# Performance work log

Hardware: AMD Instinct MI355X
Metric: run time of the kernel (lower is better)

The kernel has to match this reference:

```python
import jax, jax.numpy as jnp
import numpy as np

BATCH = 16384
NUM_CLASSES = 1000
FEA_DIM = 1024
MARGIN = 5.0


def setup_inputs() -> dict:
    key = jax.random.key(0)
    k1, k2, k3 = jax.random.split(key, 3)
    x = jax.random.normal(k1, (BATCH, FEA_DIM), dtype=jnp.float32)
    labels = jax.random.randint(k2, (BATCH,), 0, NUM_CLASSES)
    centers = jax.random.normal(k3, (NUM_CLASSES, FEA_DIM), dtype=jnp.float32)
    return {"x": x, "labels": labels, "centers": centers}


def reference(x, labels, centers):
    # Half squared euclidean distances via the GEMM expansion:
    # 0.5*||a-b||^2 = 0.5*(||a||^2 + ||b||^2 - 2 a.b)
    B = x.shape[0]
    C = centers.shape[0]
    x2 = jnp.sum(x * x, axis=1, keepdims=True)          # [B,1]
    c2 = jnp.sum(centers * centers, axis=1)             # [C]
    d_xc = 0.5 * (x2 + c2[None, :] - 2.0 * (x @ centers.T))   # [B,C]
    d_cc = 0.5 * (c2[:, None] + c2[None, :] - 2.0 * (centers @ centers.T))  # [C,C]

    is_label = labels[:, None] == jnp.arange(C)[None, :]  # [B,C] bool
    inf = jnp.float32(jnp.inf)

    # pos_center: distance to own class center
    pos = jnp.take_along_axis(d_xc, labels[:, None], axis=1)[:, 0]       # [B]
    # neg_center: min distance to any other class center
    neg = jnp.min(jnp.where(is_label, inf, d_xc), axis=1)                # [B]
    # centers term: min distance between own center and any other center
    cen = jnp.min(jnp.where(is_label, inf, d_cc[labels]), axis=1)        # [B]

    loss = jax.nn.relu(pos + MARGIN - neg) + jax.nn.relu(MARGIN + 2.0 - cen)
    return jnp.sum(loss) / B
```

## Files before the change

kernel.cpp:

```cpp
#include <hip/hip_runtime.h>
#include <hip/hip_bf16.h>
#include <stdint.h>

#define BATCH   16384
#define NCLASS  1000
#define CPAD    1024
#define FDIM    1024
#define MARGINF 5.0f

typedef __attribute__((ext_vector_type(4))) float f32x4;
typedef __attribute__((ext_vector_type(8))) short bf16x8;

__device__ __forceinline__ void gload16(const void* g, void* l) {
    __builtin_amdgcn_global_load_lds(
        (const __attribute__((address_space(1))) void*)g,
        (__attribute__((address_space(3))) void*)l, 16, 0, 0);
}

__device__ __forceinline__ unsigned short f2bf(float f) {
    __hip_bfloat16 h = __float2bfloat16(f);
    return __builtin_bit_cast(unsigned short, h);
}

__global__ void prep(const float* __restrict__ x, const float* __restrict__ c,
                     unsigned short* __restrict__ xb, unsigned short* __restrict__ cb,
                     float* __restrict__ c2) {
    const int bid = blockIdx.x;
    const int t   = threadIdx.x;
    if (bid < CPAD) {
        const int k = bid;
        if (k >= NCLASS) {
            ((ushort4*)(cb + (size_t)k * FDIM))[t] = make_ushort4(0, 0, 0, 0);
            if (t == 0) c2[k] = 1e30f;
            return;
        }
        float4 v = ((const float4*)(c + (size_t)k * FDIM))[t];
        ushort4 o;
        o.x = f2bf(v.x); o.y = f2bf(v.y); o.z = f2bf(v.z); o.w = f2bf(v.w);
        ((ushort4*)(cb + (size_t)k * FDIM))[t] = o;
        float ss = v.x * v.x + v.y * v.y + v.z * v.z + v.w * v.w;
        #pragma unroll
        for (int s = 1; s < 64; s <<= 1) ss += __shfl_xor(ss, s, 64);
        __shared__ float sred[4];
        int lane = t & 63, wid = t >> 6;
        if (lane == 0) sred[wid] = ss;
        __syncthreads();
        if (t == 0) c2[k] = sred[0] + sred[1] + sred[2] + sred[3];
    } else {
        const int n4 = BATCH * FDIM / 4;
        int i = (bid - CPAD) * 256 + t;
        const int stride = 2048 * 256;
        #pragma unroll
        for (int it = 0; it < 8; ++it, i += stride) {
            if (i < n4) {
                float4 v = ((const float4*)x)[i];
                ushort4 o;
                o.x = f2bf(v.x); o.y = f2bf(v.y); o.z = f2bf(v.z); o.w = f2bf(v.w);
                ((ushort4*)xb)[i] = o;
            }
        }
    }
}

__launch_bounds__(256, 5)
__global__ void gemm_min(const unsigned short* __restrict__ xb,
                         const unsigned short* __restrict__ cb,
                         const float* __restrict__ c2,
                         const int* __restrict__ labels,
                         float* __restrict__ pmin,
                         float* __restrict__ cpmin,
                         float* __restrict__ pos)
{
    constexpr int BM = 128, BK = 64, KTOT = 1024, NCT = 8;
    __shared__ __align__(16) char sA[BM * BK * 2];
    __shared__ __align__(16) char sB[BM * BK * 2];

    const int bid  = blockIdx.x;
    const bool cc  = (bid >= 1024);
    const int bx   = cc ? (bid - 1024) & 7 : bid & 127;
    const int by   = cc ? (bid - 1024) >> 3 : bid >> 7;

    const int t    = threadIdx.x;
    const int lane = t & 63;
    const int wave = t >> 6;
    const int wrow = wave >> 1, wcol = wave & 1;
    const int lo4  = lane & 15, hi2 = lane >> 4;

    const int rowBase = bx * BM;
    const int colBase = by * BM;
    const unsigned short* A = cc ? cb : xb;
    float* pout = cc ? cpmin : pmin;

    f32x4 acc[4][4];
    #pragma unroll
    for (int m = 0; m < 4; m++)
        #pragma unroll
        for (int n = 0; n < 4; n++) acc[m][n] = (f32x4){0.f, 0.f, 0.f, 0.f};

    const int g_t = t & 7;
    const int r_t = t >> 3;

    for (int kt = 0; kt < KTOT / BK; ++kt) {
        __syncthreads();
        const int k0 = kt * BK;
        #pragma unroll
        for (int cch = 0; cch < 4; ++cch) {
            const int row = cch * 32 + r_t;
            const int sc  = g_t ^ (row & 7);
            const unsigned short* ga = A  + (size_t)(rowBase + row) * KTOT + k0 + sc * 8;
            const unsigned short* gb = cb + (size_t)(colBase + row) * KTOT + k0 + sc * 8;
            char* la = sA + (cch * 256 + (t & 192)) * 16;
            char* lb = sB + (cch * 256 + (t & 192)) * 16;
            gload16(ga, la);
            gload16(gb, lb);
        }
        __syncthreads();
        #pragma unroll
        for (int ks = 0; ks < 2; ++ks) {
            bf16x8 af[4], bfr[4];
            #pragma unroll
            for (int m = 0; m < 4; m++) {
                const int r    = wrow * 64 + m * 16 + lo4;
                const int slot = (ks * 4 + hi2) ^ (r & 7);
                af[m] = *(const bf16x8*)(sA + r * 128 + slot * 16);
            }
            #pragma unroll
            for (int n = 0; n < 4; n++) {
                const int r    = wcol * 64 + n * 16 + lo4;
                const int slot = (ks * 4 + hi2) ^ (r & 7);
                bfr[n] = *(const bf16x8*)(sB + r * 128 + slot * 16);
            }
            #pragma unroll
            for (int m = 0; m < 4; m++)
                #pragma unroll
                for (int n = 0; n < 4; n++)
                    acc[m][n] = __builtin_amdgcn_mfma_f32_16x16x32_bf16(af[m], bfr[n], acc[m][n], 0, 0, 0);
        }
    }

    __syncthreads();
    float* sPM = (float*)sA;

    float bias[4]; int colg[4];
    #pragma unroll
    for (int n = 0; n < 4; n++) {
        const int col = colBase + wcol * 64 + n * 16 + lo4;
        colg[n] = col;
        bias[n] = 0.5f * c2[col];
    }
    #pragma unroll
    for (int m = 0; m < 4; m++) {
        #pragma unroll
        for (int j = 0; j < 4; j++) {
            const int rloc  = wrow * 64 + m * 16 + hi2 * 4 + j;
            const int rglob = rowBase + rloc;
            const int lab   = cc ? rglob : labels[rglob];
            float vmin = 1e30f;
            #pragma unroll
            for (int n = 0; n < 4; n++) {
                float tv = acc[m][n][j] + bias[n];
                if (colg[n] == lab) {
                    if (!cc) pos[rglob] = tv;
                    tv = 1e30f;
                }
                vmin = fminf(vmin, tv);
            }
            vmin = fminf(vmin, __shfl_xor(vmin, 1, 64));
            vmin = fminf(vmin, __shfl_xor(vmin, 2, 64));
            vmin = fminf(vmin, __shfl_xor(vmin, 4, 64));
            vmin = fminf(vmin, __shfl_xor(vmin, 8, 64));
            if (lo4 == 0) sPM[wcol * BM + rloc] = vmin;
        }
    }
    __syncthreads();
    if (t < BM) {
        const float v = fminf(sPM[t], sPM[BM + t]);
        pout[(size_t)(rowBase + t) * NCT + by] = v;
    }
}

__global__ void loss_k(const float* __restrict__ pmin, const float* __restrict__ pos,
                       const int* __restrict__ labels, const float* __restrict__ cpmin,
                       const float* __restrict__ c2, float* __restrict__ out) {
    const int r = blockIdx.x * 256 + threadIdx.x;
    float neg = 1e30f;
    #pragma unroll
    for (int i = 0; i < 8; i++) neg = fminf(neg, pmin[(size_t)r * 8 + i]);
    const int lab = labels[r];
    float cmin = 1e30f;
    #pragma unroll
    for (int i = 0; i < 8; i++) cmin = fminf(cmin, cpmin[(size_t)lab * 8 + i]);
    const float cen = 0.5f * c2[lab] + cmin;
    float v = fmaxf(pos[r] + MARGINF - neg, 0.f) + fmaxf(MARGINF + 2.0f - cen, 0.f);
    #pragma unroll
    for (int s = 1; s < 64; s <<= 1) v += __shfl_xor(v, s, 64);
    __shared__ float sred[4];
    int lane = threadIdx.x & 63, wid = threadIdx.x >> 6;
    if (lane == 0) sred[wid] = v;
    __syncthreads();
    if (threadIdx.x == 0)
        atomicAdd(out, (sred[0] + sred[1] + sred[2] + sred[3]) * (1.0f / (float)BATCH));
}

extern "C" void kernel_launch(void* const* d_in, const int* in_sizes, int n_in,
                              void* d_out, int out_size, void* d_ws, size_t ws_size,
                              hipStream_t stream) {
    const float* x       = (const float*)d_in[0];
    const int*   labels  = (const int*)d_in[1];
    const float* centers = (const float*)d_in[2];
    float* out = (float*)d_out;

    char* ws = (char*)d_ws;
    size_t off = 0;
    unsigned short* xb = (unsigned short*)(ws + off); off += (size_t)BATCH * FDIM * 2;
    unsigned short* cb = (unsigned short*)(ws + off); off += (size_t)CPAD * FDIM * 2;
    float* c2    = (float*)(ws + off); off += (size_t)CPAD * 4;
    float* pmin  = (float*)(ws + off); off += (size_t)BATCH * 8 * 4;
    float* pos   = (float*)(ws + off); off += (size_t)BATCH * 4;
    float* cpmin = (float*)(ws + off); off += (size_t)CPAD * 8 * 4;

    hipMemsetAsync(out, 0, sizeof(float), stream);
    prep<<<dim3(CPAD + 2048), dim3(256), 0, stream>>>(x, centers, xb, cb, c2);
    gemm_min<<<dim3(1024 + 64), dim3(256), 0, stream>>>(xb, cb, c2, labels, pmin, cpmin, pos);
    loss_k<<<dim3(BATCH / 256), dim3(256), 0, stream>>>(pmin, pos, labels, cpmin, c2, out);
}
```

Measured before the change: 192.1 us.

## Fuse x bf16 conversion into GEMM tile loads, drop separate prep pass

Removes the standalone conversion of x to bf16 and instead loads fp32 x tiles in the GEMM, converts them to bf16 in registers, and writes them swizzled into LDS. This eliminates a full read of x plus a write and reread of the bf16 copy through HBM. In exchange, each x tile is read in fp32 eight times, once per column block, so GEMM global traffic doubles for A. The A loads also become synchronous register loads instead of async global-to-LDS loads. The occupancy hint in launch bounds is dropped.

```diff
diff --git a/kernel.cpp b/kernel.cpp
--- a/kernel.cpp
+++ b/kernel.cpp
@@ -22,48 +22,35 @@
     return __builtin_bit_cast(unsigned short, h);
 }
 
-__global__ void prep(const float* __restrict__ x, const float* __restrict__ c,
-                     unsigned short* __restrict__ xb, unsigned short* __restrict__ cb,
-                     float* __restrict__ c2) {
-    const int bid = blockIdx.x;
-    const int t   = threadIdx.x;
-    if (bid < CPAD) {
-        const int k = bid;
-        if (k >= NCLASS) {
-            ((ushort4*)(cb + (size_t)k * FDIM))[t] = make_ushort4(0, 0, 0, 0);
-            if (t == 0) c2[k] = 1e30f;
-            return;
-        }
-        float4 v = ((const float4*)(c + (size_t)k * FDIM))[t];
-        ushort4 o;
-        o.x = f2bf(v.x); o.y = f2bf(v.y); o.z = f2bf(v.z); o.w = f2bf(v.w);
-        ((ushort4*)(cb + (size_t)k * FDIM))[t] = o;
-        float ss = v.x * v.x + v.y * v.y + v.z * v.z + v.w * v.w;
-        #pragma unroll
-        for (int s = 1; s < 64; s <<= 1) ss += __shfl_xor(ss, s, 64);
-        __shared__ float sred[4];
-        int lane = t & 63, wid = t >> 6;
-        if (lane == 0) sred[wid] = ss;
-        __syncthreads();
-        if (t == 0) c2[k] = sred[0] + sred[1] + sred[2] + sred[3];
-    } else {
-        const int n4 = BATCH * FDIM / 4;
-        int i = (bid - CPAD) * 256 + t;
-        const int stride = 2048 * 256;
-        #pragma unroll
-        for (int it = 0; it < 8; ++it, i += stride) {
-            if (i < n4) {
-                float4 v = ((const float4*)x)[i];
-                ushort4 o;
-                o.x = f2bf(v.x); o.y = f2bf(v.y); o.z = f2bf(v.z); o.w = f2bf(v.w);
-                ((ushort4*)xb)[i] = o;
-            }
-        }
-    }
-}
-
-__launch_bounds__(256, 5)
-__global__ void gemm_min(const unsigned short* __restrict__ xb,
+__device__ __forceinline__ unsigned int pack2(float a, float b) {
+    return (unsigned int)f2bf(a) | ((unsigned int)f2bf(b) << 16);
+}
+
+__global__ void prep_c(const float* __restrict__ c, unsigned short* __restrict__ cb,
+                       float* __restrict__ c2) {
+    const int k = blockIdx.x;
+    const int t = threadIdx.x;
+    if (k >= NCLASS) {
+        ((ushort4*)(cb + (size_t)k * FDIM))[t] = make_ushort4(0, 0, 0, 0);
+        if (t == 0) c2[k] = 1e30f;
+        return;
+    }
+    float4 v = ((const float4*)(c + (size_t)k * FDIM))[t];
+    ushort4 o;
+    o.x = f2bf(v.x); o.y = f2bf(v.y); o.z = f2bf(v.z); o.w = f2bf(v.w);
+    ((ushort4*)(cb + (size_t)k * FDIM))[t] = o;
+    float ss = v.x * v.x + v.y * v.y + v.z * v.z + v.w * v.w;
+    #pragma unroll
+    for (int s = 1; s < 64; s <<= 1) ss += __shfl_xor(ss, s, 64);
+    __shared__ float sred[4];
+    int lane = t & 63, wid = t >> 6;
+    if (lane == 0) sred[wid] = ss;
+    __syncthreads();
+    if (t == 0) c2[k] = sred[0] + sred[1] + sred[2] + sred[3];
+}
+
+__launch_bounds__(256)
+__global__ void gemm_min(const float* __restrict__ x,
                          const unsigned short* __restrict__ cb,
                          const float* __restrict__ c2,
                          const int* __restrict__ labels,
@@ -88,7 +75,6 @@
 
     const int rowBase = bx * BM;
     const int colBase = by * BM;
-    const unsigned short* A = cc ? cb : xb;
     float* pout = cc ? cpmin : pmin;
 
     f32x4 acc[4][4];
@@ -107,12 +93,30 @@
         for (int cch = 0; cch < 4; ++cch) {
             const int row = cch * 32 + r_t;
             const int sc  = g_t ^ (row & 7);
-            const unsigned short* ga = A  + (size_t)(rowBase + row) * KTOT + k0 + sc * 8;
             const unsigned short* gb = cb + (size_t)(colBase + row) * KTOT + k0 + sc * 8;
-            char* la = sA + (cch * 256 + (t & 192)) * 16;
             char* lb = sB + (cch * 256 + (t & 192)) * 16;
-            gload16(ga, la);
             gload16(gb, lb);
+        }
+        if (!cc) {
+            #pragma unroll
+            for (int cch = 0; cch < 4; ++cch) {
+                const int row = cch * 32 + r_t;
+                const float4* gp = (const float4*)(x + (size_t)(rowBase + row) * KTOT + k0 + g_t * 8);
+                float4 v0 = gp[0], v1 = gp[1];
+                int4 pk;
+                pk.x = pack2(v0.x, v0.y); pk.y = pack2(v0.z, v0.w);
+                pk.z = pack2(v1.x, v1.y); pk.w = pack2(v1.z, v1.w);
+                *(int4*)(sA + row * 128 + (g_t ^ (row & 7)) * 16) = pk;
+            }
+        } else {
+            #pragma unroll
+            for (int cch = 0; cch < 4; ++cch) {
+                const int row = cch * 32 + r_t;
+                const int sc  = g_t ^ (row & 7);
+                const unsigned short* ga = cb + (size_t)(rowBase + row) * KTOT + k0 + sc * 8;
+                char* la = sA + (cch * 256 + (t & 192)) * 16;
+                gload16(ga, la);
+            }
         }
         __syncthreads();
         #pragma unroll
@@ -212,7 +216,6 @@
 
     char* ws = (char*)d_ws;
     size_t off = 0;
-    unsigned short* xb = (unsigned short*)(ws + off); off += (size_t)BATCH * FDIM * 2;
     unsigned short* cb = (unsigned short*)(ws + off); off += (size_t)CPAD * FDIM * 2;
     float* c2    = (float*)(ws + off); off += (size_t)CPAD * 4;
     float* pmin  = (float*)(ws + off); off += (size_t)BATCH * 8 * 4;
@@ -220,7 +223,7 @@
     float* cpmin = (float*)(ws + off); off += (size_t)CPAD * 8 * 4;
 
     hipMemsetAsync(out, 0, sizeof(float), stream);
-    prep<<<dim3(CPAD + 2048), dim3(256), 0, stream>>>(x, centers, xb, cb, c2);
-    gemm_min<<<dim3(1024 + 64), dim3(256), 0, stream>>>(xb, cb, c2, labels, pmin, cpmin, pos);
+    prep_c<<<dim3(CPAD), dim3(256), 0, stream>>>(centers, cb, c2);
+    gemm_min<<<dim3(1024 + 64), dim3(256), 0, stream>>>(x, cb, c2, labels, pmin, cpmin, pos);
     loss_k<<<dim3(BATCH / 256), dim3(256), 0, stream>>>(pmin, pos, labels, cpmin, c2, out);
 }
```

After: 162.4 us. 1.18x faster.
